# Kernel tuning notes

Measured on AMD Instinct MI355X. Metric: run time of the kernel, lower is better.

Reference implementation:

```python
import jax, jax.numpy as jnp
import numpy as np
import math

DIM = 2048
N_HEADS = 16
HEAD_DIM = DIM // N_HEADS  # 128
SEQ = 2048
EPS = 1e-5
NEG = -1e9


def get_slopes(n):
    # n is a power of 2 here (16)
    start = 2.0 ** (-2.0 ** (-(math.log2(n) - 3)))
    return [start * start ** i for i in range(n)]


def setup_inputs() -> dict:
    key = jax.random.key(0)
    ks = jax.random.split(key, 6)
    x = jax.random.normal(ks[0], (1, SEQ, DIM), dtype=jnp.float32)
    # causal additive mask (large negative above diagonal)
    causal = jnp.tril(jnp.ones((SEQ, SEQ), dtype=bool))
    mask = jnp.where(causal, 0.0, NEG).astype(jnp.float32)[None, None]
    scale_w = 0.02
    wq = jax.random.normal(ks[1], (DIM, DIM), dtype=jnp.float32) * scale_w  # [in, out]
    wk = jax.random.normal(ks[2], (DIM, DIM), dtype=jnp.float32) * scale_w
    wv = jax.random.normal(ks[3], (DIM, DIM), dtype=jnp.float32) * scale_w
    wo = jax.random.normal(ks[4], (DIM, DIM), dtype=jnp.float32) * scale_w
    # AttentionPrior params: shape_init=1, scale_init='slope' (stored as log), loc_init=0
    shape = jnp.ones((1, N_HEADS, 1, 1), dtype=jnp.float32)
    scale = jnp.log(jnp.asarray(get_slopes(N_HEADS), dtype=jnp.float32)).reshape(1, N_HEADS, 1, 1)
    loc = jnp.zeros((1, N_HEADS, 1, 1), dtype=jnp.float32)
    return {"x": x, "mask": mask, "wq": wq, "wk": wk, "wv": wv, "wo": wo,
            "shape": shape, "scale": scale, "loc": loc, "start_pos": 0}


def _prior_bias(shape, scale, loc, seqlen, start_pos):
    q_pos = jnp.arange(seqlen, dtype=jnp.float32) + start_pos
    k_pos = jnp.arange(seqlen + start_pos, dtype=jnp.float32)
    dist = (k_pos[None, :] - q_pos[:, None])[None, None]  # [1,1,S,K]
    loc_t = jnp.exp(loc) - jnp.exp(-loc)
    z = (dist - loc_t) * jnp.exp(scale)  # [1,H,S,K]
    return -(jnp.abs(z) + EPS) ** shape


def reference(x, mask, wq, wk, wv, wo, shape, scale, loc, start_pos):
    bsz, seqlen, _ = x.shape
    q = (x @ wq).reshape(bsz, seqlen, N_HEADS, HEAD_DIM)
    k = (x @ wk).reshape(bsz, seqlen, N_HEADS, HEAD_DIM)
    v = (x @ wv).reshape(bsz, seqlen, N_HEADS, HEAD_DIM)
    # start_pos=0 prefill: cache slice == current keys/values
    scores = jnp.einsum('bqhd,bkhd->bhqk', q, k) / math.sqrt(HEAD_DIM)
    scores = scores + _prior_bias(shape, scale, loc, seqlen, start_pos)
    scores = scores + mask
    probs = jax.nn.softmax(scores.astype(jnp.float32), axis=-1).astype(q.dtype)
    out = jnp.einsum('bhqk,bkhd->bqhd', probs, v).reshape(bsz, seqlen, DIM)
    return out @ wo
```

## Files before the change

kernel.cpp:

```cpp
#include <hip/hip_runtime.h>
#include <hip/hip_bf16.h>
#include <stdint.h>


typedef unsigned short u16;
typedef unsigned int u32;

using bf16x8 = __attribute__((ext_vector_type(8))) __bf16;
using f32x4  = __attribute__((ext_vector_type(4))) float;

__device__ __forceinline__ u16 f2bf(float f) {
  union { float f; u32 u; } v; v.f = f;
  u32 r = (v.u + 0x7FFFu + ((v.u >> 16) & 1u)) >> 16;
  return (u16)r;
}

__device__ __forceinline__ float bf2f(u16 h) {
  union { u32 u; float f; } v; v.u = ((u32)h) << 16; return v.f;
}

__device__ __forceinline__ void gload16(const void* g, void* l) {
  __builtin_amdgcn_global_load_lds((const __attribute__((address_space(1))) void*)g,
                                   (__attribute__((address_space(3))) void*)l, 16, 0, 0);
}

__device__ __forceinline__ int cumchunks(int qt) {
  if (qt < 8)  return qt;
  if (qt < 16) return 8 + 2 * (qt - 8);
  if (qt < 24) return 24 + 3 * (qt - 16);
  return 48 + 4 * (qt - 24);
}

__global__ __launch_bounds__(256) void convx(const float* __restrict__ x, u16* __restrict__ xb) {
  int i = blockIdx.x * 256 + threadIdx.x;
  float4 v = ((const float4*)x)[i];
  ushort4 o;
  o.x = f2bf(v.x); o.y = f2bf(v.y); o.z = f2bf(v.z); o.w = f2bf(v.w);
  ((ushort4*)xb)[i] = o;
}

__global__ __launch_bounds__(256) void transw(const float* __restrict__ wq, const float* __restrict__ wk,
                                              const float* __restrict__ wv, const float* __restrict__ wo,
                                              u16* __restrict__ wqkt, u16* __restrict__ wvt,
                                              u16* __restrict__ wot) {
  __shared__ float tile[32][33];
  const int z = blockIdx.z;
  const float* src = (z == 0) ? wq : (z == 1) ? wk : (z == 2) ? wv : wo;
  u16* dst = (z == 0) ? wqkt : (z == 1) ? (wqkt + 2048 * 2048) : (z == 2) ? wvt : wot;
  const int c0 = blockIdx.x * 32, r0 = blockIdx.y * 32;
  const int t = threadIdx.x;
  const int ci = t & 31, rj = t >> 5;
#pragma unroll
  for (int j = 0; j < 4; ++j)
    tile[rj + j * 8][ci] = src[(size_t)(r0 + rj + j * 8) * 2048 + c0 + ci];
  __syncthreads();
#pragma unroll
  for (int j = 0; j < 4; ++j) {
    int rr = rj + j * 8;
    dst[(size_t)(c0 + rr) * 2048 + r0 + ci] = f2bf(tile[ci][rr]);
  }
}

__global__ __launch_bounds__(256) void gemm_qkv(const u16* __restrict__ xb, const u16* __restrict__ wqkt,
                                                const u16* __restrict__ wvt,
                                                u16* __restrict__ qkc, u16* __restrict__ vtc) {
  __shared__ u16 lds[16384];
  int bid = blockIdx.x;
  const u16 *A, *Bt;
  u16* C;
  int N, bn, bm, scl_cols;
  if (bid < 512) { A = xb;  Bt = wqkt; C = qkc; N = 4096; bn = bid & 31; bm = bid >> 5; scl_cols = 2048; }
  else { bid -= 512; A = wvt; Bt = xb; C = vtc; N = 2048; bn = bid & 15; bm = bid >> 4; scl_cols = 0; }
  const int K = 2048;

  const int t = threadIdx.x;
  const int w = t >> 6, l = t & 63;
  const int wm = w >> 1, wn = w & 1;
  const int lrow = l & 15, lgrp = l >> 4;

  f32x4 acc[4][4] = {};

  for (int k0 = 0; k0 < K; k0 += 64) {
    if (k0) __syncthreads();
#pragma unroll
    for (int p = 0; p < 4; ++p) {
      int i = (p * 4 + w) * 64 + l;
      int r = i >> 3, u = i & 7;
      const u16* src = A + (size_t)(bm * 128 + r) * K + k0 + ((u ^ (r & 7)) << 3);
      gload16(src, (char*)lds + (p * 4 + w) * 1024);
    }
#pragma unroll
    for (int p = 0; p < 4; ++p) {
      int i = (p * 4 + w) * 64 + l;
      int r = i >> 3, u = i & 7;
      const u16* src = Bt + (size_t)(bn * 128 + r) * K + k0 + ((u ^ (r & 7)) << 3);
      gload16(src, (char*)lds + 16384 + (p * 4 + w) * 1024);
    }
    __syncthreads();

#pragma unroll
    for (int kc = 0; kc < 2; ++kc) {
      bf16x8 af[4], bfr[4];
#pragma unroll
      for (int mt = 0; mt < 4; ++mt) {
        int rho = wm * 64 + mt * 16 + lrow;
        int un = (kc * 4 + lgrp) ^ (rho & 7);
        af[mt] = *(const bf16x8*)((const char*)lds + rho * 128 + un * 16);
      }
#pragma unroll
      for (int nt = 0; nt < 4; ++nt) {
        int rho = wn * 64 + nt * 16 + lrow;
        int un = (kc * 4 + lgrp) ^ (rho & 7);
        bfr[nt] = *(const bf16x8*)((const char*)lds + 16384 + rho * 128 + un * 16);
      }
#pragma unroll
      for (int mt = 0; mt < 4; ++mt)
#pragma unroll
        for (int nt = 0; nt < 4; ++nt)
          acc[mt][nt] = __builtin_amdgcn_mfma_f32_16x16x32_bf16(af[mt], bfr[nt], acc[mt][nt], 0, 0, 0);
    }
  }

  const int row0 = bm * 128 + wm * 64;
  const int col0 = bn * 128 + wn * 64;
#pragma unroll
  for (int mt = 0; mt < 4; ++mt)
#pragma unroll
    for (int nt = 0; nt < 4; ++nt) {
      int col = col0 + nt * 16 + lrow;
      float s = (col < scl_cols) ? 0.08838834764831843f : 1.0f;
#pragma unroll
      for (int r = 0; r < 4; ++r) {
        int row = row0 + mt * 16 + lgrp * 4 + r;
        C[(size_t)row * N + col] = f2bf(acc[mt][nt][r] * s);
      }
    }
}

__global__ __launch_bounds__(256) void gemm_out(const u16* __restrict__ A, const u16* __restrict__ Bt,
                                                float* __restrict__ Cv, int M, int N, int K) {
  __shared__ u16 lds[16384];
  const int t = threadIdx.x;
  const int w = t >> 6, l = t & 63;
  const int bn = blockIdx.x, bm = blockIdx.y;
  const int wm = w >> 1, wn = w & 1;
  const int lrow = l & 15, lgrp = l >> 4;

  f32x4 acc[4][4] = {};

  for (int k0 = 0; k0 < K; k0 += 64) {
    if (k0) __syncthreads();
#pragma unroll
    for (int p = 0; p < 4; ++p) {
      int i = (p * 4 + w) * 64 + l;
      int r = i >> 3, u = i & 7;
      const u16* src = A + (size_t)(bm * 128 + r) * K + k0 + ((u ^ (r & 7)) << 3);
      gload16(src, (char*)lds + (p * 4 + w) * 1024);
    }
#pragma unroll
    for (int p = 0; p < 4; ++p) {
      int i = (p * 4 + w) * 64 + l;
      int r = i >> 3, u = i & 7;
      const u16* src = Bt + (size_t)(bn * 128 + r) * K + k0 + ((u ^ (r & 7)) << 3);
      gload16(src, (char*)lds + 16384 + (p * 4 + w) * 1024);
    }
    __syncthreads();

#pragma unroll
    for (int kc = 0; kc < 2; ++kc) {
      bf16x8 af[4], bfr[4];
#pragma unroll
      for (int mt = 0; mt < 4; ++mt) {
        int rho = wm * 64 + mt * 16 + lrow;
        int un = (kc * 4 + lgrp) ^ (rho & 7);
        af[mt] = *(const bf16x8*)((const char*)lds + rho * 128 + un * 16);
      }
#pragma unroll
      for (int nt = 0; nt < 4; ++nt) {
        int rho = wn * 64 + nt * 16 + lrow;
        int un = (kc * 4 + lgrp) ^ (rho & 7);
        bfr[nt] = *(const bf16x8*)((const char*)lds + 16384 + rho * 128 + un * 16);
      }
#pragma unroll
      for (int mt = 0; mt < 4; ++mt)
#pragma unroll
        for (int nt = 0; nt < 4; ++nt)
          acc[mt][nt] = __builtin_amdgcn_mfma_f32_16x16x32_bf16(af[mt], bfr[nt], acc[mt][nt], 0, 0, 0);
    }
  }

  const int row0 = bm * 128 + wm * 64;
  const int col0 = bn * 128 + wn * 64;
#pragma unroll
  for (int mt = 0; mt < 4; ++mt)
#pragma unroll
    for (int nt = 0; nt < 4; ++nt) {
      int col = col0 + nt * 16 + lrow;
#pragma unroll
      for (int r = 0; r < 4; ++r) {
        int row = row0 + mt * 16 + lgrp * 4 + r;
        Cv[(size_t)row * N + col] = acc[mt][nt][r];
      }
    }
}

__global__ __launch_bounds__(256) void attn_part(const u16* __restrict__ QK, const u16* __restrict__ Vt,
                                                 u16* __restrict__ Opart, float* __restrict__ Lpart,
                                                 const float* __restrict__ g_shape,
                                                 const float* __restrict__ g_scale,
                                                 const float* __restrict__ g_loc,
                                                 const int* __restrict__ g_sp) {
  __shared__ u16 k_lds[2][8192];
  __shared__ u16 v_lds[2][8192];
  __shared__ u16 p_lds[4][1152];

  const int bid = blockIdx.x;
  const int h = bid / 80;
  const int rem = bid - h * 80;
  int qt, ch;
  if (rem < 8)       { qt = rem;                 ch = 0; }
  else if (rem < 24) { int r2 = rem - 8;  qt = 8  + (r2 >> 1); ch = r2 & 1; }
  else if (rem < 48) { int r3 = rem - 24; qt = 16 + r3 / 3;    ch = r3 - 3 * (r3 / 3); }
  else               { int r4 = rem - 48; qt = 24 + (r4 >> 2); ch = r4 & 3; }
  const int pid = bid;

  const int t = threadIdx.x, w = t >> 6, l = t & 63;
  const int lrow = l & 15, lgrp = l >> 4;

  const float sh = g_shape[h];
  const float es = __expf(g_scale[h]);
  const float lcv = g_loc[h];
  const float loc_t = __expf(lcv) - __expf(-lcv);
  const int sp = g_sp[0];
  const bool shape1 = (sh == 1.0f);

  const int qbase = qt * 64 + w * 16;

  bf16x8 qf[4];
  {
    const u16* qp = QK + (size_t)(qbase + lrow) * 4096 + h * 128 + lgrp * 8;
#pragma unroll
    for (int kc = 0; kc < 4; ++kc) qf[kc] = *(const bf16x8*)(qp + kc * 32);
  }

  f32x4 o[8] = {};
  float lr[4] = {0.0f, 0.0f, 0.0f, 0.0f};

  const int kstart = ch * 8;
  const int kend = min(kstart + 8, qt + 1);

#define STAGE_TILE(buf, kt_) do {                                                        \
    const int kv0s = (kt_) * 64;                                                         \
    _Pragma("unroll")                                                                    \
    for (int p = 0; p < 4; ++p) {                                                        \
      int i = (p * 4 + w) * 64 + l;                                                      \
      int r = i >> 4, u = i & 15;                                                        \
      const u16* src = QK + (size_t)(kv0s + r) * 4096 + 2048 + h * 128 + ((u ^ (r & 7)) << 3); \
      gload16(src, (char*)k_lds[buf] + (p * 4 + w) * 1024);                              \
    }                                                                                    \
    _Pragma("unroll")                                                                    \
    for (int p = 0; p < 4; ++p) {                                                        \
      int i = (p * 4 + w) * 64 + l;                                                      \
      int r = i >> 3, u = i & 7;                                                         \
      const u16* src = Vt + (size_t)(h * 128 + r) * 2048 + kv0s + ((u ^ (r & 7)) << 3);  \
      gload16(src, (char*)v_lds[buf] + (p * 4 + w) * 1024);                              \
    }                                                                                    \
  } while (0)

  STAGE_TILE(0, kstart);
  __syncthreads();

  for (int kt = kstart; kt < kend; ++kt) {
    const int cur = (kt - kstart) & 1;
    if (kt + 1 < kend) STAGE_TILE(cur ^ 1, kt + 1);
    const int kv0 = kt * 64;

    f32x4 s4[4];
#pragma unroll
    for (int nc = 0; nc < 4; ++nc) s4[nc] = f32x4{-11.0f, -11.0f, -11.0f, -11.0f};
#pragma unroll
    for (int kc = 0; kc < 4; ++kc) {
#pragma unroll
      for (int nc = 0; nc < 4; ++nc) {
        int rho = nc * 16 + lrow;
        int un = (kc * 4 + lgrp) ^ (rho & 7);
        bf16x8 bk = *(const bf16x8*)((const char*)k_lds[cur] + rho * 256 + un * 16);
        s4[nc] = __builtin_amdgcn_mfma_f32_16x16x32_bf16(qf[kc], bk, s4[nc], 0, 0, 0);
      }
    }

    f32x4 p4[4];
    const bool need_mask = (kv0 + 63 > qbase + sp);
    if (shape1 && !need_mask) {
#pragma unroll
      for (int r = 0; r < 4; ++r) {
        const float fb = (float)(kv0 + lrow - (qbase + lgrp * 4 + r) - sp) - loc_t;
#pragma unroll
        for (int nc = 0; nc < 4; ++nc) {
          float u = fb + (float)(nc * 16);
          float p = __expf(fmaf(-es, fabsf(u), s4[nc][r]));
          p4[nc][r] = p;
          lr[r] += p;
        }
      }
    } else if (shape1) {
#pragma unroll
      for (int r = 0; r < 4; ++r) {
        const float fb = (float)(kv0 + lrow - (qbase + lgrp * 4 + r) - sp) - loc_t;
#pragma unroll
        for (int nc = 0; nc < 4; ++nc) {
          float u = fb + (float)(nc * 16);
          float p = __expf(fmaf(-es, fabsf(u), s4[nc][r]));
          p = (u + loc_t > 0.0f) ? 0.0f : p;
          p4[nc][r] = p;
          lr[r] += p;
        }
      }
    } else {
#pragma unroll
      for (int r = 0; r < 4; ++r) {
        const float fb = (float)(kv0 + lrow - (qbase + lgrp * 4 + r) - sp) - loc_t;
#pragma unroll
        for (int nc = 0; nc < 4; ++nc) {
          float u = fb + (float)(nc * 16);
          float az = fmaf(es, fabsf(u), 1e-5f);
          float p = __expf(s4[nc][r] - __powf(az, sh));
          p = (u + loc_t > 0.0f) ? 0.0f : p;
          p4[nc][r] = p;
          lr[r] += p;
        }
      }
    }

#pragma unroll
    for (int r = 0; r < 4; ++r)
#pragma unroll
      for (int nc = 0; nc < 4; ++nc)
        p_lds[w][(lgrp * 4 + r) * 72 + nc * 16 + lrow] = f2bf(p4[nc][r]);

#pragma unroll
    for (int ks = 0; ks < 2; ++ks) {
      bf16x8 pa = *(const bf16x8*)((const char*)p_lds[w] + lrow * 144 + ks * 64 + lgrp * 16);
#pragma unroll
      for (int dc = 0; dc < 8; ++dc) {
        int rho = dc * 16 + lrow;
        int un = (ks * 4 + lgrp) ^ (rho & 7);
        bf16x8 bv = *(const bf16x8*)((const char*)v_lds[cur] + rho * 128 + un * 16);
        o[dc] = __builtin_amdgcn_mfma_f32_16x16x32_bf16(pa, bv, o[dc], 0, 0, 0);
      }
    }

    __syncthreads();
  }
#undef STAGE_TILE

#pragma unroll
  for (int r = 0; r < 4; ++r)
#pragma unroll
    for (int msk = 1; msk <= 8; msk <<= 1) lr[r] += __shfl_xor(lr[r], msk);

  u16* ob = Opart + (size_t)pid * 8192;
#pragma unroll
  for (int dc = 0; dc < 8; ++dc) {
#pragma unroll
    for (int r = 0; r < 4; ++r) {
      int row = w * 16 + lgrp * 4 + r;
      ob[(size_t)row * 128 + dc * 16 + lrow] = f2bf(o[dc][r]);
    }
  }
  if (lrow == 0) {
#pragma unroll
    for (int r = 0; r < 4; ++r) {
      int row = w * 16 + lgrp * 4 + r;
      Lpart[(size_t)pid * 64 + row] = lr[r];
    }
  }
}

__global__ __launch_bounds__(256) void attn_merge(const u16* __restrict__ Opart,
                                                  const float* __restrict__ Lpart,
                                                  u16* __restrict__ AO) {
  const int bid = blockIdx.x;
  const int qt = bid & 31, h = bid >> 5;
  const int nch = (qt >> 3) + 1;
  const int base = h * 80 + cumchunks(qt);
  const int t = threadIdx.x;
  const int row = t >> 2;
  const int dseg = (t & 3) << 5;

  float acc[32] = {};
  float lstar = 0.0f;
#pragma unroll
  for (int i = 0; i < 4; ++i) {
    if (i < nch) {
      lstar += Lpart[(size_t)(base + i) * 64 + row];
      const ushort4* op = (const ushort4*)(Opart + (size_t)(base + i) * 8192 + row * 128 + dseg);
#pragma unroll
      for (int j = 0; j < 8; ++j) {
        ushort4 v = op[j];
        acc[j * 4 + 0] += bf2f(v.x); acc[j * 4 + 1] += bf2f(v.y);
        acc[j * 4 + 2] += bf2f(v.z); acc[j * 4 + 3] += bf2f(v.w);
      }
    }
  }
  const float inv = 1.0f / lstar;
  const int q_abs = qt * 64 + row;
  u16* dst = AO + (size_t)q_abs * 2048 + h * 128 + dseg;
#pragma unroll
  for (int j = 0; j < 8; ++j) {
    ushort4 ov;
    ov.x = f2bf(acc[j * 4 + 0] * inv); ov.y = f2bf(acc[j * 4 + 1] * inv);
    ov.z = f2bf(acc[j * 4 + 2] * inv); ov.w = f2bf(acc[j * 4 + 3] * inv);
    *(ushort4*)(dst + j * 4) = ov;
  }
}

extern "C" void kernel_launch(void* const* d_in, const int* in_sizes, int n_in,
                              void* d_out, int out_size, void* d_ws, size_t ws_size,
                              hipStream_t stream) {
  const float* x   = (const float*)d_in[0];
  const float* wq  = (const float*)d_in[2];
  const float* wk  = (const float*)d_in[3];
  const float* wv  = (const float*)d_in[4];
  const float* wo  = (const float*)d_in[5];
  const float* shp = (const float*)d_in[6];
  const float* scl = (const float*)d_in[7];
  const float* loc = (const float*)d_in[8];
  const int*   sp  = (const int*)d_in[9];

  char* ws = (char*)d_ws;
  u16*   xb    = (u16*)(ws);
  u16*   wqkt  = (u16*)(ws + (size_t)( 8u << 20));
  u16*   wvt   = (u16*)(ws + (size_t)(24u << 20));
  u16*   opart = (u16*)(ws);
  u16*   wot   = (u16*)(ws + (size_t)(40u << 20));
  u16*   qk    = (u16*)(ws + (size_t)(48u << 20));
  u16*   vt    = (u16*)(ws + (size_t)(64u << 20));
  u16*   ao    = (u16*)(ws + (size_t)(72u << 20));
  float* lpart = (float*)(ws + (size_t)(80u << 20));

  hipLaunchKernelGGL(convx, dim3(4096), dim3(256), 0, stream, x, xb);
  hipLaunchKernelGGL(transw, dim3(64, 64, 4), dim3(256), 0, stream, wq, wk, wv, wo, wqkt, wvt, wot);
  hipLaunchKernelGGL(gemm_qkv, dim3(768), dim3(256), 0, stream, xb, wqkt, wvt, qk, vt);
  hipLaunchKernelGGL(attn_part, dim3(1280), dim3(256), 0, stream,
                     qk, vt, opart, lpart, shp, scl, loc, sp);
  hipLaunchKernelGGL(attn_merge, dim3(512), dim3(256), 0, stream, opart, lpart, ao);
  hipLaunchKernelGGL(gemm_out, dim3(16, 16), dim3(256), 0, stream,
                     ao, wot, (float*)d_out, 2048, 2048, 2048);
}
```

Measured before the change: 177.7 us.

## Split-K output GEMM into two partials and remap block IDs across XCDs

The output projection is split along K into two halves, doubling the block count from 256 to 512 so more compute units are busy. Each half writes a bf16 partial, and a new combine kernel adds the two into the fp32 output. Block indices in gemm_qkv, attn_part and the new GEMM are also remapped so that consecutive logical blocks are spread across the eight XCDs, which is meant to improve L2 locality. The cost is an extra kernel launch, extra partial-buffer traffic, and the precision loss of rounding the partials to bf16 before summing.

```diff
diff --git a/kernel.cpp b/kernel.cpp
--- a/kernel.cpp
+++ b/kernel.cpp
@@ -65,7 +65,8 @@
                                                 const u16* __restrict__ wvt,
                                                 u16* __restrict__ qkc, u16* __restrict__ vtc) {
   __shared__ u16 lds[16384];
-  int bid = blockIdx.x;
+  const int raw = blockIdx.x;
+  int bid = (raw & 7) * 96 + (raw >> 3);
   const u16 *A, *Bt;
   u16* C;
   int N, bn, bm, scl_cols;
@@ -137,19 +138,26 @@
     }
 }
 
-__global__ __launch_bounds__(256) void gemm_out(const u16* __restrict__ A, const u16* __restrict__ Bt,
-                                                float* __restrict__ Cv, int M, int N, int K) {
+__global__ __launch_bounds__(256) void gemm_outk(const u16* __restrict__ A, const u16* __restrict__ Bt,
+                                                 u16* __restrict__ P0, u16* __restrict__ P1) {
   __shared__ u16 lds[16384];
+  const int raw = blockIdx.x;
+  const int b = (raw & 7) * 64 + (raw >> 3);
+  const int z = b >> 8;
+  const int bn = b & 15, bm = (b >> 4) & 15;
+  u16* C = z ? P1 : P0;
+  const int K = 2048;
+  const int kbeg = z * 1024, kend = kbeg + 1024;
+
   const int t = threadIdx.x;
   const int w = t >> 6, l = t & 63;
-  const int bn = blockIdx.x, bm = blockIdx.y;
   const int wm = w >> 1, wn = w & 1;
   const int lrow = l & 15, lgrp = l >> 4;
 
   f32x4 acc[4][4] = {};
 
-  for (int k0 = 0; k0 < K; k0 += 64) {
-    if (k0) __syncthreads();
+  for (int k0 = kbeg; k0 < kend; k0 += 64) {
+    if (k0 != kbeg) __syncthreads();
 #pragma unroll
     for (int p = 0; p < 4; ++p) {
       int i = (p * 4 + w) * 64 + l;
@@ -199,9 +207,23 @@
 #pragma unroll
       for (int r = 0; r < 4; ++r) {
         int row = row0 + mt * 16 + lgrp * 4 + r;
-        Cv[(size_t)row * N + col] = acc[mt][nt][r];
-      }
-    }
+        C[(size_t)row * 2048 + col] = f2bf(acc[mt][nt][r]);
+      }
+    }
+}
+
+__global__ __launch_bounds__(256) void combine_out(const u16* __restrict__ P0, const u16* __restrict__ P1,
+                                                   float* __restrict__ out) {
+  const int i = blockIdx.x * 256 + threadIdx.x;
+  uint4 a = ((const uint4*)P0)[i];
+  uint4 b = ((const uint4*)P1)[i];
+  float4 o0, o1;
+  o0.x = bf2f(a.x & 0xFFFF) + bf2f(b.x & 0xFFFF); o0.y = bf2f(a.x >> 16) + bf2f(b.x >> 16);
+  o0.z = bf2f(a.y & 0xFFFF) + bf2f(b.y & 0xFFFF); o0.w = bf2f(a.y >> 16) + bf2f(b.y >> 16);
+  o1.x = bf2f(a.z & 0xFFFF) + bf2f(b.z & 0xFFFF); o1.y = bf2f(a.z >> 16) + bf2f(b.z >> 16);
+  o1.z = bf2f(a.w & 0xFFFF) + bf2f(b.w & 0xFFFF); o1.w = bf2f(a.w >> 16) + bf2f(b.w >> 16);
+  ((float4*)out)[i * 2]     = o0;
+  ((float4*)out)[i * 2 + 1] = o1;
 }
 
 __global__ __launch_bounds__(256) void attn_part(const u16* __restrict__ QK, const u16* __restrict__ Vt,
@@ -214,7 +236,8 @@
   __shared__ u16 v_lds[2][8192];
   __shared__ u16 p_lds[4][1152];
 
-  const int bid = blockIdx.x;
+  const int raw = blockIdx.x;
+  const int bid = (raw & 7) * 160 + (raw >> 3);
   const int h = bid / 80;
   const int rem = bid - h * 80;
   int qt, ch;
@@ -435,6 +458,8 @@
   u16*   opart = (u16*)(ws);
   u16*   wot   = (u16*)(ws + (size_t)(40u << 20));
   u16*   qk    = (u16*)(ws + (size_t)(48u << 20));
+  u16*   pc0   = (u16*)(ws + (size_t)(48u << 20));
+  u16*   pc1   = (u16*)(ws + (size_t)(56u << 20));
   u16*   vt    = (u16*)(ws + (size_t)(64u << 20));
   u16*   ao    = (u16*)(ws + (size_t)(72u << 20));
   float* lpart = (float*)(ws + (size_t)(80u << 20));
@@ -445,6 +470,6 @@
   hipLaunchKernelGGL(attn_part, dim3(1280), dim3(256), 0, stream,
                      qk, vt, opart, lpart, shp, scl, loc, sp);
   hipLaunchKernelGGL(attn_merge, dim3(512), dim3(256), 0, stream, opart, lpart, ao);
-  hipLaunchKernelGGL(gemm_out, dim3(16, 16), dim3(256), 0, stream,
-                     ao, wot, (float*)d_out, 2048, 2048, 2048);
-}
+  hipLaunchKernelGGL(gemm_outk, dim3(512), dim3(256), 0, stream, ao, wot, pc0, pc1);
+  hipLaunchKernelGGL(combine_out, dim3(2048), dim3(256), 0, stream, pc0, pc1, (float*)d_out);
+}
```

Result: faster. 172.8 us (-2.8%).
